# Kernel tuning notes

Hardware: AMD Instinct MI355X
Metric: run time of the kernel (lower is better)

Reference implementation:

```python
import jax, jax.numpy as jnp
import numpy as np

EPS = 1e-3  # kernel epsilon used in Performer generalized kernel
B, H, N, D, M = 1, 8, 1024, 64, 128  # batch, heads, seq, dim_heads, nb_features


def _gaussian_orthogonal_matrix(m, d, seed=0):
    # GaussianOrthogonalRandomMatrix with scaling=0: stacked QR blocks, rows
    # rescaled by chi-distributed norms of gaussian d-vectors.
    rng = np.random.default_rng(seed)
    blocks = []
    for _ in range(m // d):
        g = rng.standard_normal((d, d))
        qmat, _ = np.linalg.qr(g)
        blocks.append(qmat.T)
    proj = np.concatenate(blocks, axis=0)  # [m, d], orthonormal rows per block
    mult = np.linalg.norm(rng.standard_normal((m, d)), axis=1)  # chi norms
    return (mult[:, None] * proj).astype(np.float32)


def setup_inputs() -> dict:
    key = jax.random.key(0)
    kq, kk, kv = jax.random.split(key, 3)
    q = jax.random.normal(kq, (B, H, N, D), dtype=jnp.float32)
    k = jax.random.normal(kk, (B, H, N, D), dtype=jnp.float32)
    v = jax.random.normal(kv, (B, H, N, D), dtype=jnp.float32)
    proj = jnp.asarray(_gaussian_orthogonal_matrix(M, D))
    return {"q": q, "k": k, "v": v, "proj": proj}


def _generalized_kernel(x, proj):
    # kernel_fn(relu)( (x / d**0.25) @ proj^T ) + eps
    normalizer = 1.0 / (x.shape[-1] ** 0.25)
    xp = jnp.einsum('bhnd,md->bhnm', x * normalizer, proj)
    return jax.nn.relu(xp) + EPS


def reference(q, k, v, proj):
    qp = _generalized_kernel(q, proj)  # [B,H,N,M]
    kp = _generalized_kernel(k, proj)  # [B,H,N,M]
    # causal linear attention
    k_cumsum = jnp.cumsum(kp, axis=-2)                              # [B,H,N,M]
    context = jnp.einsum('bhnm,bhne->bhnme', kp, v)                 # [B,H,N,M,D]
    context = jnp.cumsum(context, axis=-3)                          # prefix sums over n
    context = context / k_cumsum[..., None]                         # normalize
    out = jnp.einsum('bhnme,bhnm->bhne', context, qp)               # [B,H,N,D]
    return out
```

## Files before the change

### kernel.cpp

```cpp
#include <hip/hip_runtime.h>

static constexpr int H = 8, N = 1024, D = 64, M = 128;
static constexpr float EPS = 1e-3f;
static constexpr float NORM = 0.35355339059327373f;

typedef __attribute__((ext_vector_type(8))) short short8;
typedef __attribute__((ext_vector_type(4))) float f32x4;

__device__ inline unsigned short f2bf(float x) {
    unsigned u = __float_as_uint(x);
    return (unsigned short)((u + 0x7fffu + ((u >> 16) & 1u)) >> 16);
}
__device__ inline float bf2f(unsigned short u) {
    return __uint_as_float(((unsigned)u) << 16);
}
__device__ inline ushort4 pack4(float4 g) {
    return (ushort4){f2bf(g.x), f2bf(g.y), f2bf(g.z), f2bf(g.w)};
}

__global__ __launch_bounds__(512) void k_projg(const float* __restrict__ q,
                                               const float* __restrict__ k,
                                               const float* __restrict__ proj,
                                               const float* __restrict__ v,
                                               unsigned short* __restrict__ qpb,
                                               unsigned short* __restrict__ kpb,
                                               unsigned short* __restrict__ Gpb,
                                               float* __restrict__ kpart) {
    __shared__ __align__(16) short smem[30208];
    short* projb = smem;
    short* xb = smem + 9216;
    short* obuf = smem + 13824;
    short* kpT = smem + 22528;
    short* vT = smem + 27648;
    const int tid = threadIdx.x;
    const int rblk = blockIdx.x;
    const int h = blockIdx.y;
    const int rowbase = h * N + rblk * 32;
    const int lane = tid & 63, wv = tid >> 6;
    const int rt = wv & 3, mh = wv >> 2;
    const int fr = lane & 15, fq = lane >> 4;

    for (int i4 = tid; i4 < 2048; i4 += 512) {
        int m = i4 >> 4, dq = i4 & 15;
        *(ushort4*)&projb[m * 72 + dq * 4] = pack4(*(const float4*)&proj[i4 * 4]);
    }
    {
        int r = tid >> 4, dq = tid & 15;
        float4 g = *(const float4*)&q[(rowbase + r) * D + dq * 4];
        g.x *= NORM; g.y *= NORM; g.z *= NORM; g.w *= NORM;
        *(ushort4*)&xb[r * 72 + dq * 4] = pack4(g);
        float4 gk = *(const float4*)&k[(rowbase + r) * D + dq * 4];
        gk.x *= NORM; gk.y *= NORM; gk.z *= NORM; gk.w *= NORM;
        *(ushort4*)&xb[(32 + r) * 72 + dq * 4] = pack4(gk);
        int rv = tid & 31, e4 = (tid >> 5) * 4;
        float4 gv = *(const float4*)&v[(rowbase + rv) * D + e4];
        vT[(e4 + 0) * 40 + rv] = (short)f2bf(gv.x);
        vT[(e4 + 1) * 40 + rv] = (short)f2bf(gv.y);
        vT[(e4 + 2) * 40 + rv] = (short)f2bf(gv.z);
        vT[(e4 + 3) * 40 + rv] = (short)f2bf(gv.w);
    }
    __syncthreads();

    f32x4 accp[4];
#pragma unroll
    for (int i = 0; i < 4; i++) accp[i] = (f32x4){0.f, 0.f, 0.f, 0.f};
#pragma unroll
    for (int kt = 0; kt < 2; kt++) {
        short8 a = *(const short8*)&xb[(16 * rt + fr) * 72 + kt * 32 + fq * 8];
#pragma unroll
        for (int i = 0; i < 4; i++) {
            const int mt = mh * 4 + i;
            short8 bb = *(const short8*)&projb[(16 * mt + fr) * 72 + kt * 32 + fq * 8];
            accp[i] = __builtin_amdgcn_mfma_f32_16x16x32_bf16(a, bb, accp[i], 0, 0, 0);
        }
    }
#pragma unroll
    for (int i = 0; i < 4; i++) {
        const int mt = mh * 4 + i;
#pragma unroll
        for (int reg = 0; reg < 4; reg++) {
            const int r = 16 * rt + fq * 4 + reg;
            const int m = 16 * mt + fr;
            unsigned short bv = f2bf(fmaxf(accp[i][reg], 0.f) + EPS);
            obuf[r * 136 + m] = (short)bv;
            if (rt >= 2) kpT[m * 40 + (r - 32)] = (short)bv;
        }
    }
    __syncthreads();

    for (int i = tid; i < 2048; i += 512) {
        int r = i >> 5, cu = i & 31;
        ushort4 val = *(const ushort4*)&obuf[r * 136 + cu * 4];
        unsigned short* g = (r < 32) ? &qpb[(rowbase + r) * M + cu * 4]
                                     : &kpb[(rowbase + r - 32) * M + cu * 4];
        *(ushort4*)g = val;
    }
    const int gb = h * 32 + rblk;
    if (tid < 128) {
        float ks = 0.f;
#pragma unroll 8
        for (int r = 0; r < 32; r++) ks += bf2f((unsigned short)kpT[tid * 40 + r]);
        kpart[gb * M + tid] = ks;
    }
    __syncthreads();

    f32x4 gacc[4];
#pragma unroll
    for (int et = 0; et < 4; et++) gacc[et] = (f32x4){0.f, 0.f, 0.f, 0.f};
    {
        short8 a = *(const short8*)&kpT[(16 * wv + fr) * 40 + fq * 8];
#pragma unroll
        for (int et = 0; et < 4; et++) {
            short8 bb = *(const short8*)&vT[(16 * et + fr) * 40 + fq * 8];
            gacc[et] = __builtin_amdgcn_mfma_f32_16x16x32_bf16(a, bb, gacc[et], 0, 0, 0);
        }
    }
#pragma unroll
    for (int et = 0; et < 4; et++)
#pragma unroll
        for (int reg = 0; reg < 4; reg++) {
            const int m = 16 * wv + fq * 4 + reg;
            obuf[m * 68 + 16 * et + fr] = (short)f2bf(gacc[et][reg]);
        }
    __syncthreads();
    for (int i = tid; i < 2048; i += 512) {
        int m = i >> 4, e4 = (i & 15) * 4;
        *(ushort4*)&Gpb[(gb * M + m) * D + e4] = *(const ushort4*)&obuf[m * 68 + e4];
    }
}

__global__ __launch_bounds__(256) void k_prefix(const float* __restrict__ kpart,
                                                const unsigned short* __restrict__ Gpb,
                                                float* __restrict__ zpre,
                                                unsigned short* __restrict__ S0pre) {
    const int h = blockIdx.x >> 3, oct = blockIdx.x & 7;
    const int tid = threadIdx.x;
    const int eb = oct * 1024 + tid * 4;
    float a0 = 0.f, a1 = 0.f, a2 = 0.f, a3 = 0.f;
#pragma unroll 4
    for (int s = 0; s < 32; s++) {
        ushort4 w = {f2bf(a0), f2bf(a1), f2bf(a2), f2bf(a3)};
        *(ushort4*)&S0pre[(h * 32 + s) * (M * D) + eb] = w;
        ushort4 g = *(const ushort4*)&Gpb[(h * 32 + s) * (M * D) + eb];
        a0 += bf2f(g.x);
        a1 += bf2f(g.y);
        a2 += bf2f(g.z);
        a3 += bf2f(g.w);
    }
    if (oct == 0 && tid < 128) {
        float vals[32];
#pragma unroll
        for (int s = 0; s < 32; s++) vals[s] = kpart[(h * 32 + s) * M + tid];
        float z = 0.f;
#pragma unroll
        for (int s = 0; s < 32; s++) {
            zpre[(h * 32 + s) * M + tid] = z;
            z += vals[s];
        }
    }
}

__global__ __launch_bounds__(512) void k_attn(const unsigned short* __restrict__ qpb,
                                              const unsigned short* __restrict__ kpb,
                                              const float* __restrict__ zpre,
                                              const unsigned short* __restrict__ S0pre,
                                              const float* __restrict__ v,
                                              float* __restrict__ out) {
    __shared__ __align__(16) short smem[25600];
    short* bufW = smem;
    short* bufK = smem + 4352;
    short* bufQ = smem + 8704;
    short* s0t  = smem + 13056;
    short* vT   = smem + 21760;
    short* bufP = smem + 24320;
    const int tid = threadIdx.x;
    const int b = blockIdx.x;
    const int h = b >> 5, s = b & 31;
    const int rowstart = h * N + s * 32;
    const int lane = tid & 63, wv = tid >> 6;
    const int rt = wv & 1, js = wv >> 1;
    const int fr = lane & 15, fq = lane >> 4;

    {
        const unsigned int* srck = (const unsigned int*)kpb;
        const unsigned int* srcq = (const unsigned int*)qpb;
        for (int i = tid; i < 2048; i += 512) {
            int j = i >> 6, mu = i & 63;
            ((unsigned int*)&bufK[j * 136])[mu] = srck[(rowstart + j) * 64 + mu];
            ((unsigned int*)&bufQ[j * 136])[mu] = srcq[(rowstart + j) * 64 + mu];
        }
    }
    {
        const int pm = tid >> 2, peb = (tid & 3) * 16;
        const unsigned short* src = &S0pre[(h * 32 + s) * (M * D) + pm * D + peb];
        short8 s0a = *(const short8*)&src[0];
        short8 s0b = *(const short8*)&src[8];
#pragma unroll
        for (int j = 0; j < 8; j++) {
            s0t[(peb + j) * 136 + pm] = s0a[j];
            s0t[(peb + 8 + j) * 136 + pm] = s0b[j];
        }
    }
    {
        const int j = tid >> 4, e4 = (tid & 15) * 4;
        float4 gv = *(const float4*)&v[(rowstart + j) * D + e4];
        vT[(e4 + 0) * 40 + j] = (short)f2bf(gv.x);
        vT[(e4 + 1) * 40 + j] = (short)f2bf(gv.y);
        vT[(e4 + 2) * 40 + j] = (short)f2bf(gv.z);
        vT[(e4 + 3) * 40 + j] = (short)f2bf(gv.w);
    }
    float zinit = 0.f;
    if (tid < 128) zinit = zpre[(h * 32 + s) * M + tid];
    __syncthreads();

    if (tid < 128) {
        const int m = tid;
        float z = zinit;
#pragma unroll 8
        for (int r = 0; r < 32; r++) {
            z += bf2f((unsigned short)bufK[r * 136 + m]);
            bufW[r * 136 + m] = (short)f2bf(
                bf2f((unsigned short)bufQ[r * 136 + m]) * __builtin_amdgcn_rcpf(z));
        }
    }
    __syncthreads();

    f32x4 acc2 = (f32x4){0.f, 0.f, 0.f, 0.f};
#pragma unroll
    for (int kt = 0; kt < 4; kt++) {
        short8 a = *(const short8*)&bufW[(16 * rt + fr) * 136 + kt * 32 + fq * 8];
        short8 bb = *(const short8*)&s0t[(16 * js + fr) * 136 + kt * 32 + fq * 8];
        acc2 = __builtin_amdgcn_mfma_f32_16x16x32_bf16(a, bb, acc2, 0, 0, 0);
    }
    if (wv < 4) {
        const int jt = wv >> 1;
        f32x4 acc1 = (f32x4){0.f, 0.f, 0.f, 0.f};
#pragma unroll
        for (int kt = 0; kt < 4; kt++) {
            short8 a = *(const short8*)&bufW[(16 * rt + fr) * 136 + kt * 32 + fq * 8];
            short8 bb = *(const short8*)&bufK[(16 * jt + fr) * 136 + kt * 32 + fq * 8];
            acc1 = __builtin_amdgcn_mfma_f32_16x16x32_bf16(a, bb, acc1, 0, 0, 0);
        }
        const int j = 16 * jt + fr;
#pragma unroll
        for (int reg = 0; reg < 4; reg++) {
            const int nloc = 16 * rt + fq * 4 + reg;
            float val = (j <= nloc) ? acc1[reg] : 0.f;
            bufP[nloc * 40 + j] = (short)f2bf(val);
        }
    }
    __syncthreads();

    {
        short8 a = *(const short8*)&bufP[(16 * rt + fr) * 40 + fq * 8];
        short8 bb = *(const short8*)&vT[(16 * js + fr) * 40 + fq * 8];
        acc2 = __builtin_amdgcn_mfma_f32_16x16x32_bf16(a, bb, acc2, 0, 0, 0);
    }

#pragma unroll
    for (int reg = 0; reg < 4; reg++) {
        out[(rowstart + 16 * rt + fq * 4 + reg) * D + 16 * js + fr] = acc2[reg];
    }
}

extern "C" void kernel_launch(void* const* d_in, const int* in_sizes, int n_in,
                              void* d_out, int out_size, void* d_ws, size_t ws_size,
                              hipStream_t stream) {
    const float* q = (const float*)d_in[0];
    const float* k = (const float*)d_in[1];
    const float* v = (const float*)d_in[2];
    const float* proj = (const float*)d_in[3];
    float* out = (float*)d_out;

    float* ws = (float*)d_ws;
    float* kpart = ws;
    unsigned short* qpb = (unsigned short*)(kpart + H * 32 * M);
    unsigned short* kpb = qpb + H * N * M;
    unsigned short* Gpb = kpb + H * N * M;
    float* zpre = (float*)(Gpb + H * 32 * M * D);
    unsigned short* S0pre = (unsigned short*)(zpre + H * 32 * M);

    k_projg<<<dim3(32, H), 512, 0, stream>>>(q, k, proj, v, qpb, kpb, Gpb,
                                             kpart);
    k_prefix<<<dim3(64), 256, 0, stream>>>(kpart, Gpb, zpre, S0pre);
    k_attn<<<dim3(H * 32), 512, 0, stream>>>(qpb, kpb, zpre, S0pre, v, out);
}
```

Before: 80.30 us.

## Fuse three kernels into one persistent kernel with grid barriers

Merges the projection, prefix-sum and attention kernels into a single 256-block launch separated by software grid barriers built on atomic counters, which are zeroed by a memset before the launch. The goal is to remove the launch gaps and tail effects between the three kernels. The prefix stage is redistributed over all 256 blocks, using scalar rather than vectorised accesses. It relies on all 256 blocks being co-resident, which should hold on this GPU; if they were not, the barriers would deadlock. It also adds a memset and atomic spin-wait overhead.

```diff
diff --git a/kernel.cpp b/kernel.cpp
--- a/kernel.cpp
+++ b/kernel.cpp
@@ -1,6 +1,7 @@
 #include <hip/hip_runtime.h>
 
 static constexpr int H = 8, N = 1024, D = 64, M = 128;
+static constexpr unsigned NBLK = 256;
 static constexpr float EPS = 1e-3f;
 static constexpr float NORM = 0.35355339059327373f;
 
@@ -18,248 +19,262 @@
     return (ushort4){f2bf(g.x), f2bf(g.y), f2bf(g.z), f2bf(g.w)};
 }
 
-__global__ __launch_bounds__(512) void k_projg(const float* __restrict__ q,
-                                               const float* __restrict__ k,
-                                               const float* __restrict__ proj,
-                                               const float* __restrict__ v,
-                                               unsigned short* __restrict__ qpb,
-                                               unsigned short* __restrict__ kpb,
-                                               unsigned short* __restrict__ Gpb,
-                                               float* __restrict__ kpart) {
-    __shared__ __align__(16) short smem[30208];
-    short* projb = smem;
-    short* xb = smem + 9216;
-    short* obuf = smem + 13824;
-    short* kpT = smem + 22528;
-    short* vT = smem + 27648;
-    const int tid = threadIdx.x;
-    const int rblk = blockIdx.x;
-    const int h = blockIdx.y;
-    const int rowbase = h * N + rblk * 32;
-    const int lane = tid & 63, wv = tid >> 6;
-    const int rt = wv & 3, mh = wv >> 2;
-    const int fr = lane & 15, fq = lane >> 4;
-
-    for (int i4 = tid; i4 < 2048; i4 += 512) {
-        int m = i4 >> 4, dq = i4 & 15;
-        *(ushort4*)&projb[m * 72 + dq * 4] = pack4(*(const float4*)&proj[i4 * 4]);
-    }
-    {
-        int r = tid >> 4, dq = tid & 15;
-        float4 g = *(const float4*)&q[(rowbase + r) * D + dq * 4];
-        g.x *= NORM; g.y *= NORM; g.z *= NORM; g.w *= NORM;
-        *(ushort4*)&xb[r * 72 + dq * 4] = pack4(g);
-        float4 gk = *(const float4*)&k[(rowbase + r) * D + dq * 4];
-        gk.x *= NORM; gk.y *= NORM; gk.z *= NORM; gk.w *= NORM;
-        *(ushort4*)&xb[(32 + r) * 72 + dq * 4] = pack4(gk);
-        int rv = tid & 31, e4 = (tid >> 5) * 4;
-        float4 gv = *(const float4*)&v[(rowbase + rv) * D + e4];
-        vT[(e4 + 0) * 40 + rv] = (short)f2bf(gv.x);
-        vT[(e4 + 1) * 40 + rv] = (short)f2bf(gv.y);
-        vT[(e4 + 2) * 40 + rv] = (short)f2bf(gv.z);
-        vT[(e4 + 3) * 40 + rv] = (short)f2bf(gv.w);
+__device__ inline void grid_barrier(unsigned* cnt) {
+    __syncthreads();
+    if (threadIdx.x == 0) {
+        __threadfence();
+        atomicAdd(cnt, 1u);
+        while (__hip_atomic_load(cnt, __ATOMIC_RELAXED,
+                                 __HIP_MEMORY_SCOPE_AGENT) < NBLK) {
+            __builtin_amdgcn_s_sleep(2);
+        }
+        __threadfence();
     }
     __syncthreads();
-
-    f32x4 accp[4];
-#pragma unroll
-    for (int i = 0; i < 4; i++) accp[i] = (f32x4){0.f, 0.f, 0.f, 0.f};
-#pragma unroll
-    for (int kt = 0; kt < 2; kt++) {
-        short8 a = *(const short8*)&xb[(16 * rt + fr) * 72 + kt * 32 + fq * 8];
+}
+
+__global__ __launch_bounds__(512) void k_fused(
+    const float* __restrict__ q, const float* __restrict__ k,
+    const float* __restrict__ proj, const float* __restrict__ v,
+    unsigned short* __restrict__ qpb, unsigned short* __restrict__ kpb,
+    unsigned short* __restrict__ Gpb, float* __restrict__ kpart,
+    float* __restrict__ zpre, unsigned short* __restrict__ S0pre,
+    float* __restrict__ out, unsigned* __restrict__ bar) {
+    __shared__ __align__(16) short smem[30208];
+    const int tid = threadIdx.x;
+    const int b = blockIdx.x;
+
+    {
+        short* projb = smem;
+        short* xb = smem + 9216;
+        short* obuf = smem + 13824;
+        short* kpT = smem + 22528;
+        short* vT = smem + 27648;
+        const int rblk = b & 31;
+        const int h = b >> 5;
+        const int rowbase = h * N + rblk * 32;
+        const int lane = tid & 63, wv = tid >> 6;
+        const int rt = wv & 3, mh = wv >> 2;
+        const int fr = lane & 15, fq = lane >> 4;
+
+        for (int i4 = tid; i4 < 2048; i4 += 512) {
+            int m = i4 >> 4, dq = i4 & 15;
+            *(ushort4*)&projb[m * 72 + dq * 4] =
+                pack4(*(const float4*)&proj[i4 * 4]);
+        }
+        {
+            int r = tid >> 4, dq = tid & 15;
+            float4 g = *(const float4*)&q[(rowbase + r) * D + dq * 4];
+            g.x *= NORM; g.y *= NORM; g.z *= NORM; g.w *= NORM;
+            *(ushort4*)&xb[r * 72 + dq * 4] = pack4(g);
+            float4 gk = *(const float4*)&k[(rowbase + r) * D + dq * 4];
+            gk.x *= NORM; gk.y *= NORM; gk.z *= NORM; gk.w *= NORM;
+            *(ushort4*)&xb[(32 + r) * 72 + dq * 4] = pack4(gk);
+            int rv = tid & 31, e4 = (tid >> 5) * 4;
+            float4 gv = *(const float4*)&v[(rowbase + rv) * D + e4];
+            vT[(e4 + 0) * 40 + rv] = (short)f2bf(gv.x);
+            vT[(e4 + 1) * 40 + rv] = (short)f2bf(gv.y);
+            vT[(e4 + 2) * 40 + rv] = (short)f2bf(gv.z);
+            vT[(e4 + 3) * 40 + rv] = (short)f2bf(gv.w);
+        }
+        __syncthreads();
+
+        f32x4 accp[4];
+#pragma unroll
+        for (int i = 0; i < 4; i++) accp[i] = (f32x4){0.f, 0.f, 0.f, 0.f};
+#pragma unroll
+        for (int kt = 0; kt < 2; kt++) {
+            short8 a = *(const short8*)&xb[(16 * rt + fr) * 72 + kt * 32 + fq * 8];
+#pragma unroll
+            for (int i = 0; i < 4; i++) {
+                const int mt = mh * 4 + i;
+                short8 bb =
+                    *(const short8*)&projb[(16 * mt + fr) * 72 + kt * 32 + fq * 8];
+                accp[i] =
+                    __builtin_amdgcn_mfma_f32_16x16x32_bf16(a, bb, accp[i], 0, 0, 0);
+            }
+        }
 #pragma unroll
         for (int i = 0; i < 4; i++) {
             const int mt = mh * 4 + i;
-            short8 bb = *(const short8*)&projb[(16 * mt + fr) * 72 + kt * 32 + fq * 8];
-            accp[i] = __builtin_amdgcn_mfma_f32_16x16x32_bf16(a, bb, accp[i], 0, 0, 0);
+#pragma unroll
+            for (int reg = 0; reg < 4; reg++) {
+                const int r = 16 * rt + fq * 4 + reg;
+                const int m = 16 * mt + fr;
+                unsigned short bv = f2bf(fmaxf(accp[i][reg], 0.f) + EPS);
+                obuf[r * 136 + m] = (short)bv;
+                if (rt >= 2) kpT[m * 40 + (r - 32)] = (short)bv;
+            }
+        }
+        __syncthreads();
+
+        for (int i = tid; i < 2048; i += 512) {
+            int r = i >> 5, cu = i & 31;
+            ushort4 val = *(const ushort4*)&obuf[r * 136 + cu * 4];
+            unsigned short* g = (r < 32) ? &qpb[(rowbase + r) * M + cu * 4]
+                                         : &kpb[(rowbase + r - 32) * M + cu * 4];
+            *(ushort4*)g = val;
+        }
+        const int gb = h * 32 + rblk;
+        if (tid < 128) {
+            float ks = 0.f;
+#pragma unroll 8
+            for (int r = 0; r < 32; r++)
+                ks += bf2f((unsigned short)kpT[tid * 40 + r]);
+            kpart[gb * M + tid] = ks;
+        }
+        __syncthreads();
+
+        f32x4 gacc[4];
+#pragma unroll
+        for (int et = 0; et < 4; et++) gacc[et] = (f32x4){0.f, 0.f, 0.f, 0.f};
+        {
+            short8 a = *(const short8*)&kpT[(16 * wv + fr) * 40 + fq * 8];
+#pragma unroll
+            for (int et = 0; et < 4; et++) {
+                short8 bb = *(const short8*)&vT[(16 * et + fr) * 40 + fq * 8];
+                gacc[et] =
+                    __builtin_amdgcn_mfma_f32_16x16x32_bf16(a, bb, gacc[et], 0, 0, 0);
+            }
+        }
+#pragma unroll
+        for (int et = 0; et < 4; et++)
+#pragma unroll
+            for (int reg = 0; reg < 4; reg++) {
+                const int m = 16 * wv + fq * 4 + reg;
+                obuf[m * 68 + 16 * et + fr] = (short)f2bf(gacc[et][reg]);
+            }
+        __syncthreads();
+        for (int i = tid; i < 2048; i += 512) {
+            int m = i >> 4, e4 = (i & 15) * 4;
+            *(ushort4*)&Gpb[(gb * M + m) * D + e4] =
+                *(const ushort4*)&obuf[m * 68 + e4];
         }
     }
-#pragma unroll
-    for (int i = 0; i < 4; i++) {
-        const int mt = mh * 4 + i;
-#pragma unroll
-        for (int reg = 0; reg < 4; reg++) {
-            const int r = 16 * rt + fq * 4 + reg;
-            const int m = 16 * mt + fr;
-            unsigned short bv = f2bf(fmaxf(accp[i][reg], 0.f) + EPS);
-            obuf[r * 136 + m] = (short)bv;
-            if (rt >= 2) kpT[m * 40 + (r - 32)] = (short)bv;
+    grid_barrier(&bar[0]);
+
+    {
+        const int h = b >> 5, seg = b & 31;
+        if (tid < 256) {
+            const int eb = seg * 256 + tid;
+            float a = 0.f;
+#pragma unroll 8
+            for (int s = 0; s < 32; s++) {
+                S0pre[(h * 32 + s) * (M * D) + eb] = f2bf(a);
+                a += bf2f(Gpb[(h * 32 + s) * (M * D) + eb]);
+            }
+        }
+        if (seg == 0 && tid < 128) {
+            float z = 0.f;
+#pragma unroll 8
+            for (int s = 0; s < 32; s++) {
+                zpre[(h * 32 + s) * M + tid] = z;
+                z += kpart[(h * 32 + s) * M + tid];
+            }
         }
     }
-    __syncthreads();
-
-    for (int i = tid; i < 2048; i += 512) {
-        int r = i >> 5, cu = i & 31;
-        ushort4 val = *(const ushort4*)&obuf[r * 136 + cu * 4];
-        unsigned short* g = (r < 32) ? &qpb[(rowbase + r) * M + cu * 4]
-                                     : &kpb[(rowbase + r - 32) * M + cu * 4];
-        *(ushort4*)g = val;
-    }
-    const int gb = h * 32 + rblk;
-    if (tid < 128) {
-        float ks = 0.f;
+    grid_barrier(&bar[1]);
+
+    {
+        short* bufW = smem;
+        short* bufK = smem + 4352;
+        short* bufQ = smem + 8704;
+        short* s0t = smem + 13056;
+        short* vT = smem + 21760;
+        short* bufP = smem + 24320;
+        const int h = b >> 5, s = b & 31;
+        const int rowstart = h * N + s * 32;
+        const int lane = tid & 63, wv = tid >> 6;
+        const int rt = wv & 1, js = wv >> 1;
+        const int fr = lane & 15, fq = lane >> 4;
+
+        {
+            const unsigned int* srck = (const unsigned int*)kpb;
+            const unsigned int* srcq = (const unsigned int*)qpb;
+            for (int i = tid; i < 2048; i += 512) {
+                int j = i >> 6, mu = i & 63;
+                ((unsigned int*)&bufK[j * 136])[mu] =
+                    srck[(rowstart + j) * 64 + mu];
+                ((unsigned int*)&bufQ[j * 136])[mu] =
+                    srcq[(rowstart + j) * 64 + mu];
+            }
+        }
+        {
+            const int pm = tid >> 2, peb = (tid & 3) * 16;
+            const unsigned short* src =
+                &S0pre[(h * 32 + s) * (M * D) + pm * D + peb];
+            short8 s0a = *(const short8*)&src[0];
+            short8 s0b = *(const short8*)&src[8];
+#pragma unroll
+            for (int j = 0; j < 8; j++) {
+                s0t[(peb + j) * 136 + pm] = s0a[j];
+                s0t[(peb + 8 + j) * 136 + pm] = s0b[j];
+            }
+        }
+        {
+            const int j = tid >> 4, e4 = (tid & 15) * 4;
+            float4 gv = *(const float4*)&v[(rowstart + j) * D + e4];
+            vT[(e4 + 0) * 40 + j] = (short)f2bf(gv.x);
+            vT[(e4 + 1) * 40 + j] = (short)f2bf(gv.y);
+            vT[(e4 + 2) * 40 + j] = (short)f2bf(gv.z);
+            vT[(e4 + 3) * 40 + j] = (short)f2bf(gv.w);
+        }
+        float zinit = 0.f;
+        if (tid < 128) zinit = zpre[(h * 32 + s) * M + tid];
+        __syncthreads();
+
+        if (tid < 128) {
+            const int m = tid;
+            float z = zinit;
 #pragma unroll 8
-        for (int r = 0; r < 32; r++) ks += bf2f((unsigned short)kpT[tid * 40 + r]);
-        kpart[gb * M + tid] = ks;
-    }
-    __syncthreads();
-
-    f32x4 gacc[4];
-#pragma unroll
-    for (int et = 0; et < 4; et++) gacc[et] = (f32x4){0.f, 0.f, 0.f, 0.f};
-    {
-        short8 a = *(const short8*)&kpT[(16 * wv + fr) * 40 + fq * 8];
-#pragma unroll
-        for (int et = 0; et < 4; et++) {
-            short8 bb = *(const short8*)&vT[(16 * et + fr) * 40 + fq * 8];
-            gacc[et] = __builtin_amdgcn_mfma_f32_16x16x32_bf16(a, bb, gacc[et], 0, 0, 0);
-        }
-    }
-#pragma unroll
-    for (int et = 0; et < 4; et++)
-#pragma unroll
-        for (int reg = 0; reg < 4; reg++) {
-            const int m = 16 * wv + fq * 4 + reg;
-            obuf[m * 68 + 16 * et + fr] = (short)f2bf(gacc[et][reg]);
-        }
-    __syncthreads();
-    for (int i = tid; i < 2048; i += 512) {
-        int m = i >> 4, e4 = (i & 15) * 4;
-        *(ushort4*)&Gpb[(gb * M + m) * D + e4] = *(const ushort4*)&obuf[m * 68 + e4];
-    }
-}
-
-__global__ __launch_bounds__(256) void k_prefix(const float* __restrict__ kpart,
-                                                const unsigned short* __restrict__ Gpb,
-                                                float* __restrict__ zpre,
-                                                unsigned short* __restrict__ S0pre) {
-    const int h = blockIdx.x >> 3, oct = blockIdx.x & 7;
-    const int tid = threadIdx.x;
-    const int eb = oct * 1024 + tid * 4;
-    float a0 = 0.f, a1 = 0.f, a2 = 0.f, a3 = 0.f;
-#pragma unroll 4
-    for (int s = 0; s < 32; s++) {
-        ushort4 w = {f2bf(a0), f2bf(a1), f2bf(a2), f2bf(a3)};
-        *(ushort4*)&S0pre[(h * 32 + s) * (M * D) + eb] = w;
-        ushort4 g = *(const ushort4*)&Gpb[(h * 32 + s) * (M * D) + eb];
-        a0 += bf2f(g.x);
-        a1 += bf2f(g.y);
-        a2 += bf2f(g.z);
-        a3 += bf2f(g.w);
-    }
-    if (oct == 0 && tid < 128) {
-        float vals[32];
-#pragma unroll
-        for (int s = 0; s < 32; s++) vals[s] = kpart[(h * 32 + s) * M + tid];
-        float z = 0.f;
-#pragma unroll
-        for (int s = 0; s < 32; s++) {
-            zpre[(h * 32 + s) * M + tid] = z;
-            z += vals[s];
-        }
-    }
-}
-
-__global__ __launch_bounds__(512) void k_attn(const unsigned short* __restrict__ qpb,
-                                              const unsigned short* __restrict__ kpb,
-                                              const float* __restrict__ zpre,
-                                              const unsigned short* __restrict__ S0pre,
-                                              const float* __restrict__ v,
-                                              float* __restrict__ out) {
-    __shared__ __align__(16) short smem[25600];
-    short* bufW = smem;
-    short* bufK = smem + 4352;
-    short* bufQ = smem + 8704;
-    short* s0t  = smem + 13056;
-    short* vT   = smem + 21760;
-    short* bufP = smem + 24320;
-    const int tid = threadIdx.x;
-    const int b = blockIdx.x;
-    const int h = b >> 5, s = b & 31;
-    const int rowstart = h * N + s * 32;
-    const int lane = tid & 63, wv = tid >> 6;
-    const int rt = wv & 1, js = wv >> 1;
-    const int fr = lane & 15, fq = lane >> 4;
-
-    {
-        const unsigned int* srck = (const unsigned int*)kpb;
-        const unsigned int* srcq = (const unsigned int*)qpb;
-        for (int i = tid; i < 2048; i += 512) {
-            int j = i >> 6, mu = i & 63;
-            ((unsigned int*)&bufK[j * 136])[mu] = srck[(rowstart + j) * 64 + mu];
-            ((unsigned int*)&bufQ[j * 136])[mu] = srcq[(rowstart + j) * 64 + mu];
-        }
-    }
-    {
-        const int pm = tid >> 2, peb = (tid & 3) * 16;
-        const unsigned short* src = &S0pre[(h * 32 + s) * (M * D) + pm * D + peb];
-        short8 s0a = *(const short8*)&src[0];
-        short8 s0b = *(const short8*)&src[8];
-#pragma unroll
-        for (int j = 0; j < 8; j++) {
-            s0t[(peb + j) * 136 + pm] = s0a[j];
-            s0t[(peb + 8 + j) * 136 + pm] = s0b[j];
-        }
-    }
-    {
-        const int j = tid >> 4, e4 = (tid & 15) * 4;
-        float4 gv = *(const float4*)&v[(rowstart + j) * D + e4];
-        vT[(e4 + 0) * 40 + j] = (short)f2bf(gv.x);
-        vT[(e4 + 1) * 40 + j] = (short)f2bf(gv.y);
-        vT[(e4 + 2) * 40 + j] = (short)f2bf(gv.z);
-        vT[(e4 + 3) * 40 + j] = (short)f2bf(gv.w);
-    }
-    float zinit = 0.f;
-    if (tid < 128) zinit = zpre[(h * 32 + s) * M + tid];
-    __syncthreads();
-
-    if (tid < 128) {
-        const int m = tid;
-        float z = zinit;
-#pragma unroll 8
-        for (int r = 0; r < 32; r++) {
-            z += bf2f((unsigned short)bufK[r * 136 + m]);
-            bufW[r * 136 + m] = (short)f2bf(
-                bf2f((unsigned short)bufQ[r * 136 + m]) * __builtin_amdgcn_rcpf(z));
-        }
-    }
-    __syncthreads();
-
-    f32x4 acc2 = (f32x4){0.f, 0.f, 0.f, 0.f};
-#pragma unroll
-    for (int kt = 0; kt < 4; kt++) {
-        short8 a = *(const short8*)&bufW[(16 * rt + fr) * 136 + kt * 32 + fq * 8];
-        short8 bb = *(const short8*)&s0t[(16 * js + fr) * 136 + kt * 32 + fq * 8];
-        acc2 = __builtin_amdgcn_mfma_f32_16x16x32_bf16(a, bb, acc2, 0, 0, 0);
-    }
-    if (wv < 4) {
-        const int jt = wv >> 1;
-        f32x4 acc1 = (f32x4){0.f, 0.f, 0.f, 0.f};
+            for (int r = 0; r < 32; r++) {
+                z += bf2f((unsigned short)bufK[r * 136 + m]);
+                bufW[r * 136 + m] = (short)f2bf(
+                    bf2f((unsigned short)bufQ[r * 136 + m]) *
+                    __builtin_amdgcn_rcpf(z));
+            }
+        }
+        __syncthreads();
+
+        f32x4 acc2 = (f32x4){0.f, 0.f, 0.f, 0.f};
 #pragma unroll
         for (int kt = 0; kt < 4; kt++) {
             short8 a = *(const short8*)&bufW[(16 * rt + fr) * 136 + kt * 32 + fq * 8];
-            short8 bb = *(const short8*)&bufK[(16 * jt + fr) * 136 + kt * 32 + fq * 8];
-            acc1 = __builtin_amdgcn_mfma_f32_16x16x32_bf16(a, bb, acc1, 0, 0, 0);
-        }
-        const int j = 16 * jt + fr;
+            short8 bb = *(const short8*)&s0t[(16 * js + fr) * 136 + kt * 32 + fq * 8];
+            acc2 = __builtin_amdgcn_mfma_f32_16x16x32_bf16(a, bb, acc2, 0, 0, 0);
+        }
+        if (wv < 4) {
+            const int jt = wv >> 1;
+            f32x4 acc1 = (f32x4){0.f, 0.f, 0.f, 0.f};
+#pragma unroll
+            for (int kt = 0; kt < 4; kt++) {
+                short8 a =
+                    *(const short8*)&bufW[(16 * rt + fr) * 136 + kt * 32 + fq * 8];
+                short8 bb =
+                    *(const short8*)&bufK[(16 * jt + fr) * 136 + kt * 32 + fq * 8];
+                acc1 = __builtin_amdgcn_mfma_f32_16x16x32_bf16(a, bb, acc1, 0, 0, 0);
+            }
+            const int j = 16 * jt + fr;
+#pragma unroll
+            for (int reg = 0; reg < 4; reg++) {
+                const int nloc = 16 * rt + fq * 4 + reg;
+                float val = (j <= nloc) ? acc1[reg] : 0.f;
+                bufP[nloc * 40 + j] = (short)f2bf(val);
+            }
+        }
+        __syncthreads();
+
+        {
+            short8 a = *(const short8*)&bufP[(16 * rt + fr) * 40 + fq * 8];
+            short8 bb = *(const short8*)&vT[(16 * js + fr) * 40 + fq * 8];
+            acc2 = __builtin_amdgcn_mfma_f32_16x16x32_bf16(a, bb, acc2, 0, 0, 0);
+        }
+
 #pragma unroll
         for (int reg = 0; reg < 4; reg++) {
-            const int nloc = 16 * rt + fq * 4 + reg;
-            float val = (j <= nloc) ? acc1[reg] : 0.f;
-            bufP[nloc * 40 + j] = (short)f2bf(val);
-        }
-    }
-    __syncthreads();
-
-    {
-        short8 a = *(const short8*)&bufP[(16 * rt + fr) * 40 + fq * 8];
-        short8 bb = *(const short8*)&vT[(16 * js + fr) * 40 + fq * 8];
-        acc2 = __builtin_amdgcn_mfma_f32_16x16x32_bf16(a, bb, acc2, 0, 0, 0);
-    }
-
-#pragma unroll
-    for (int reg = 0; reg < 4; reg++) {
-        out[(rowstart + 16 * rt + fq * 4 + reg) * D + 16 * js + fr] = acc2[reg];
+            out[(rowstart + 16 * rt + fq * 4 + reg) * D + 16 * js + fr] =
+                acc2[reg];
+        }
     }
 }
 
@@ -272,16 +287,15 @@
     const float* proj = (const float*)d_in[3];
     float* out = (float*)d_out;
 
-    float* ws = (float*)d_ws;
-    float* kpart = ws;
+    unsigned* bar = (unsigned*)d_ws;
+    float* kpart = (float*)((char*)d_ws + 64);
     unsigned short* qpb = (unsigned short*)(kpart + H * 32 * M);
     unsigned short* kpb = qpb + H * N * M;
     unsigned short* Gpb = kpb + H * N * M;
     float* zpre = (float*)(Gpb + H * 32 * M * D);
     unsigned short* S0pre = (unsigned short*)(zpre + H * 32 * M);
 
-    k_projg<<<dim3(32, H), 512, 0, stream>>>(q, k, proj, v, qpb, kpb, Gpb,
-                                             kpart);
-    k_prefix<<<dim3(64), 256, 0, stream>>>(kpart, Gpb, zpre, S0pre);
-    k_attn<<<dim3(H * 32), 512, 0, stream>>>(qpb, kpb, zpre, S0pre, v, out);
-}
+    hipMemsetAsync(d_ws, 0, 64, stream);
+    k_fused<<<dim3(NBLK), dim3(512), 0, stream>>>(q, k, proj, v, qpb, kpb, Gpb,
+                                                  kpart, zpre, S0pre, out, bar);
+}
```

Result: slower. 124.6 us (+55.2%).

## Batch global loads before LDS stores and widen prefix-scan grid

Applied to the files above, without the earlier changes.

In the projection and attention kernels, all global loads are now issued up front before any shared-memory stores, so their latencies overlap instead of serialising. The qp/kp write-out and load paths use 16-byte short8 accesses in place of 8-byte or 4-byte ones. The prefix kernel goes from 64 to 256 blocks, each thread scanning one element with scalar bf16 accesses, which gives more parallelism in exchange for narrower memory transactions. The z prefix now reads kpart inside the loop instead of preloading it into a register array.

```diff
diff --git a/kernel.cpp b/kernel.cpp
--- a/kernel.cpp
+++ b/kernel.cpp
@@ -40,24 +40,24 @@
     const int rt = wv & 3, mh = wv >> 2;
     const int fr = lane & 15, fq = lane >> 4;
 
-    for (int i4 = tid; i4 < 2048; i4 += 512) {
-        int m = i4 >> 4, dq = i4 & 15;
-        *(ushort4*)&projb[m * 72 + dq * 4] = pack4(*(const float4*)&proj[i4 * 4]);
-    }
     {
         int r = tid >> 4, dq = tid & 15;
         float4 g = *(const float4*)&q[(rowbase + r) * D + dq * 4];
+        float4 gk = *(const float4*)&k[(rowbase + r) * D + dq * 4];
+        int rv = tid & 31, e4 = (tid >> 5) * 4;
+        float4 gv = *(const float4*)&v[(rowbase + rv) * D + e4];
         g.x *= NORM; g.y *= NORM; g.z *= NORM; g.w *= NORM;
         *(ushort4*)&xb[r * 72 + dq * 4] = pack4(g);
-        float4 gk = *(const float4*)&k[(rowbase + r) * D + dq * 4];
         gk.x *= NORM; gk.y *= NORM; gk.z *= NORM; gk.w *= NORM;
         *(ushort4*)&xb[(32 + r) * 72 + dq * 4] = pack4(gk);
-        int rv = tid & 31, e4 = (tid >> 5) * 4;
-        float4 gv = *(const float4*)&v[(rowbase + rv) * D + e4];
         vT[(e4 + 0) * 40 + rv] = (short)f2bf(gv.x);
         vT[(e4 + 1) * 40 + rv] = (short)f2bf(gv.y);
         vT[(e4 + 2) * 40 + rv] = (short)f2bf(gv.z);
         vT[(e4 + 3) * 40 + rv] = (short)f2bf(gv.w);
+    }
+    for (int i4 = tid; i4 < 2048; i4 += 512) {
+        int m = i4 >> 4, dq = i4 & 15;
+        *(ushort4*)&projb[m * 72 + dq * 4] = pack4(*(const float4*)&proj[i4 * 4]);
     }
     __syncthreads();
 
@@ -88,12 +88,12 @@
     }
     __syncthreads();
 
-    for (int i = tid; i < 2048; i += 512) {
-        int r = i >> 5, cu = i & 31;
-        ushort4 val = *(const ushort4*)&obuf[r * 136 + cu * 4];
-        unsigned short* g = (r < 32) ? &qpb[(rowbase + r) * M + cu * 4]
-                                     : &kpb[(rowbase + r - 32) * M + cu * 4];
-        *(ushort4*)g = val;
+    for (int i = tid; i < 1024; i += 512) {
+        int r = i >> 4, cu8 = i & 15;
+        short8 val = *(const short8*)&obuf[r * 136 + cu8 * 8];
+        unsigned short* g = (r < 32) ? &qpb[(rowbase + r) * M + cu8 * 8]
+                                     : &kpb[(rowbase + r - 32) * M + cu8 * 8];
+        *(short8*)g = val;
     }
     const int gb = h * 32 + rblk;
     if (tid < 128) {
@@ -133,29 +133,21 @@
                                                 const unsigned short* __restrict__ Gpb,
                                                 float* __restrict__ zpre,
                                                 unsigned short* __restrict__ S0pre) {
-    const int h = blockIdx.x >> 3, oct = blockIdx.x & 7;
+    const int h = blockIdx.x >> 5, seg = blockIdx.x & 31;
     const int tid = threadIdx.x;
-    const int eb = oct * 1024 + tid * 4;
-    float a0 = 0.f, a1 = 0.f, a2 = 0.f, a3 = 0.f;
-#pragma unroll 4
+    const int eb = seg * 256 + tid;
+    float a = 0.f;
+#pragma unroll 8
     for (int s = 0; s < 32; s++) {
-        ushort4 w = {f2bf(a0), f2bf(a1), f2bf(a2), f2bf(a3)};
-        *(ushort4*)&S0pre[(h * 32 + s) * (M * D) + eb] = w;
-        ushort4 g = *(const ushort4*)&Gpb[(h * 32 + s) * (M * D) + eb];
-        a0 += bf2f(g.x);
-        a1 += bf2f(g.y);
-        a2 += bf2f(g.z);
-        a3 += bf2f(g.w);
-    }
-    if (oct == 0 && tid < 128) {
-        float vals[32];
-#pragma unroll
-        for (int s = 0; s < 32; s++) vals[s] = kpart[(h * 32 + s) * M + tid];
+        S0pre[(h * 32 + s) * (M * D) + eb] = f2bf(a);
+        a += bf2f(Gpb[(h * 32 + s) * (M * D) + eb]);
+    }
+    if (seg == 0 && tid < 128) {
         float z = 0.f;
-#pragma unroll
+#pragma unroll 8
         for (int s = 0; s < 32; s++) {
             zpre[(h * 32 + s) * M + tid] = z;
-            z += vals[s];
+            z += kpart[(h * 32 + s) * M + tid];
         }
     }
 }
@@ -181,36 +173,29 @@
     const int rt = wv & 1, js = wv >> 1;
     const int fr = lane & 15, fq = lane >> 4;
 
-    {
-        const unsigned int* srck = (const unsigned int*)kpb;
-        const unsigned int* srcq = (const unsigned int*)qpb;
-        for (int i = tid; i < 2048; i += 512) {
-            int j = i >> 6, mu = i & 63;
-            ((unsigned int*)&bufK[j * 136])[mu] = srck[(rowstart + j) * 64 + mu];
-            ((unsigned int*)&bufQ[j * 136])[mu] = srcq[(rowstart + j) * 64 + mu];
-        }
-    }
-    {
-        const int pm = tid >> 2, peb = (tid & 3) * 16;
-        const unsigned short* src = &S0pre[(h * 32 + s) * (M * D) + pm * D + peb];
-        short8 s0a = *(const short8*)&src[0];
-        short8 s0b = *(const short8*)&src[8];
-#pragma unroll
-        for (int j = 0; j < 8; j++) {
-            s0t[(peb + j) * 136 + pm] = s0a[j];
-            s0t[(peb + 8 + j) * 136 + pm] = s0b[j];
-        }
-    }
-    {
-        const int j = tid >> 4, e4 = (tid & 15) * 4;
-        float4 gv = *(const float4*)&v[(rowstart + j) * D + e4];
-        vT[(e4 + 0) * 40 + j] = (short)f2bf(gv.x);
-        vT[(e4 + 1) * 40 + j] = (short)f2bf(gv.y);
-        vT[(e4 + 2) * 40 + j] = (short)f2bf(gv.z);
-        vT[(e4 + 3) * 40 + j] = (short)f2bf(gv.w);
-    }
+    const int sj = tid >> 4, smu = tid & 15;
+    short8 kpre = *(const short8*)&kpb[(rowstart + sj) * M + smu * 8];
+    short8 qpre = *(const short8*)&qpb[(rowstart + sj) * M + smu * 8];
+    const int pm = tid >> 2, peb = (tid & 3) * 16;
+    const unsigned short* s0src = &S0pre[(h * 32 + s) * (M * D) + pm * D + peb];
+    short8 s0a = *(const short8*)&s0src[0];
+    short8 s0b = *(const short8*)&s0src[8];
+    const int ve4 = (tid & 15) * 4;
+    float4 gv = *(const float4*)&v[(rowstart + sj) * D + ve4];
     float zinit = 0.f;
     if (tid < 128) zinit = zpre[(h * 32 + s) * M + tid];
+
+    *(short8*)&bufK[sj * 136 + smu * 8] = kpre;
+    *(short8*)&bufQ[sj * 136 + smu * 8] = qpre;
+#pragma unroll
+    for (int j = 0; j < 8; j++) {
+        s0t[(peb + j) * 136 + pm] = s0a[j];
+        s0t[(peb + 8 + j) * 136 + pm] = s0b[j];
+    }
+    vT[(ve4 + 0) * 40 + sj] = (short)f2bf(gv.x);
+    vT[(ve4 + 1) * 40 + sj] = (short)f2bf(gv.y);
+    vT[(ve4 + 2) * 40 + sj] = (short)f2bf(gv.z);
+    vT[(ve4 + 3) * 40 + sj] = (short)f2bf(gv.w);
     __syncthreads();
 
     if (tid < 128) {
@@ -282,6 +267,6 @@
 
     k_projg<<<dim3(32, H), 512, 0, stream>>>(q, k, proj, v, qpb, kpb, Gpb,
                                              kpart);
-    k_prefix<<<dim3(64), 256, 0, stream>>>(kpart, Gpb, zpre, S0pre);
+    k_prefix<<<dim3(256), 256, 0, stream>>>(kpart, Gpb, zpre, S0pre);
     k_attn<<<dim3(H * 32), 512, 0, stream>>>(qpb, kpb, zpre, S0pre, v, out);
 }
```

Result: faster. 77.21 us (-3.9%).
